# Kernel tuning notes

Measured on AMD Instinct MI355X. Metric: run time of the kernel, lower is better.

The kernel has to match this reference:

```python
import jax, jax.numpy as jnp
import numpy as np

B_, H_, N_, L_ = 4, 512, 64, 2048  # batch, d_model, d_state/2 (conj pairs), seq len


def setup_inputs() -> dict:
    key = jax.random.key(0)
    ks = jax.random.split(key, 8)
    x = jax.random.normal(ks[0], (B_, H_, L_), jnp.float32)
    ln_w = jnp.ones((H_,), jnp.float32)
    ln_b = jnp.zeros((H_,), jnp.float32)
    # S4D-style init: dt log-uniform in [1e-3, 1e-1], A = -1/2 + i*pi*n (S4D-Lin)
    log_dt = jax.random.uniform(ks[1], (H_,), jnp.float32) * (np.log(0.1) - np.log(0.001)) + np.log(0.001)
    log_A_real = jnp.broadcast_to(jnp.log(jnp.float32(0.5)), (H_, N_))
    A_imag = jnp.broadcast_to(np.pi * jnp.arange(N_, dtype=np.float32), (H_, N_))
    B_re = jnp.ones((H_, N_), jnp.float32)
    B_im = jnp.zeros((H_, N_), jnp.float32)
    # 2 kernel channels for bidirectional
    C_re = jax.random.normal(ks[2], (2, H_, N_), jnp.float32) * (0.5 ** 0.5)
    C_im = jax.random.normal(ks[3], (2, H_, N_), jnp.float32) * (0.5 ** 0.5)
    D = jax.random.normal(ks[4], (H_,), jnp.float32)
    W_out = jax.random.normal(ks[5], (H_, H_), jnp.float32) / np.sqrt(H_)
    b_out = jnp.zeros((H_,), jnp.float32)
    return dict(x=x, ln_w=ln_w, ln_b=ln_b, log_dt=log_dt, log_A_real=log_A_real,
                A_imag=A_imag, B_re=B_re, B_im=B_im, C_re=C_re, C_im=C_im,
                D=D, W_out=W_out, b_out=b_out)


def _s4_layer(x, ln_w, ln_b, log_dt, log_A_real, A_imag, B_re, B_im, C_re, C_im, D, W_out, b_out):
    Bb, H, L = x.shape
    # ---- pre-norm LayerNorm over channel dim (module transposes to (B,L,H)) ----
    zt = x.transpose(0, 2, 1)                          # (B, L, H)
    mu = zt.mean(-1, keepdims=True)
    var = jnp.mean((zt - mu) ** 2, -1, keepdims=True)
    zt = (zt - mu) * jax.lax.rsqrt(var + 1e-5) * ln_w + ln_b
    z = zt.transpose(0, 2, 1)                          # (B, H, L)
    # ---- S4 diagonal SSM kernel, ZOH discretization, 2 channels (bidirectional) ----
    dt = jnp.exp(log_dt)[:, None]                      # (H, 1)
    A = -jnp.exp(log_A_real) + 1j * A_imag             # (H, N)
    dtA = A * dt                                       # (H, N)
    dB = (B_re + 1j * B_im) * (jnp.exp(dtA) - 1.0) / A # (H, N) discretized B
    CB = (C_re + 1j * C_im) * dB                       # (2, H, N)
    V = jnp.exp(dtA[:, :, None] * jnp.arange(L))       # (H, N, L) Vandermonde exp(l*dt*A)
    k = 2.0 * jnp.real(jnp.einsum('chn,hnl->chl', CB, V))  # (2, H, L)
    # ---- bidirectional: causal + flipped anticausal kernel, length 2L ----
    zpad = jnp.zeros_like(k[0])
    kb = jnp.concatenate([k[0], zpad], -1) + jnp.concatenate([zpad, k[1][:, ::-1]], -1)  # (H, 2L)
    # ---- FFT convolution ----
    k_f = jnp.fft.rfft(kb, n=2 * L)                    # (H, L+1)
    u_f = jnp.fft.rfft(z, n=2 * L)                     # (B, H, L+1)
    y = jnp.fft.irfft(u_f * k_f, n=2 * L)[..., :L]     # (B, H, L)
    y = y + z * D[:, None]                             # skip connection D*u
    y = jax.nn.gelu(y)                                 # default S4 activation
    y = jnp.einsum('oh,bhl->bol', W_out, y) + b_out[:, None]  # output linear (Conv1d k=1)
    return y + x                                       # residual of S4Layer


def reference(x, ln_w, ln_b, log_dt, log_A_real, A_imag, B_re, B_im, C_re, C_im, D, W_out, b_out):
    return _s4_layer(x, ln_w, ln_b, log_dt, log_A_real, A_imag, B_re, B_im, C_re, C_im, D, W_out, b_out)
```

## Files before the change

### kernel.cpp

```cpp
#include <hip/hip_runtime.h>
#include <math.h>

#define Bq 4
#define Hq 512
#define Nq 64
#define Lq 2048
#define PARAM (Hq*Nq)
#define T 64
#define NC (Lq/T)
#define NCOL 256

__global__ void prep_kernel(const float* __restrict__ log_dt,
                            const float* __restrict__ log_A_real,
                            const float* __restrict__ A_imag,
                            const float* __restrict__ B_re, const float* __restrict__ B_im,
                            const float* __restrict__ C_re, const float* __restrict__ C_im,
                            float* __restrict__ a0, float* __restrict__ b0,
                            float* __restrict__ a1, float* __restrict__ b1,
                            float* __restrict__ pw) {
    int idx = blockIdx.x * blockDim.x + threadIdx.x;
    if (idx >= PARAM) return;
    int h = idx >> 6, n = idx & 63;
    float dt = expf(log_dt[h]);
    float Ar = -expf(log_A_real[idx]);
    float Ai = A_imag[idx];
    float er = expf(Ar * dt);
    float wr = er * cosf(Ai * dt);
    float wi = er * sinf(Ai * dt);
    float mr = wr - 1.0f, mi = wi;
    float den = Ar * Ar + Ai * Ai;
    float qr = (mr * Ar + mi * Ai) / den;
    float qi = (mi * Ar - mr * Ai) / den;
    float Br = B_re[idx], Bi = B_im[idx];
    float dBr = Br * qr - Bi * qi;
    float dBi = Br * qi + Bi * qr;
    float cr = C_re[idx], ci = C_im[idx];
    a0[idx] =  2.0f * (cr * dBr - ci * dBi);
    b0[idx] = -2.0f * (cr * dBi + ci * dBr);
    cr = C_re[PARAM + idx]; ci = C_im[PARAM + idx];
    a1[idx] =  2.0f * (cr * dBr - ci * dBi);
    b1[idx] = -2.0f * (cr * dBi + ci * dBr);
    float c = 1.f, s = 0.f;
    float* base = pw + (size_t)h * 65 * 128 + 2 * n;
    for (int d = 0; d <= 64; ++d) {
        *(float2*)(base + (size_t)d * 128) = float2{c, s};
        float nc = c * wr - s * wi;
        float ns = c * wi + s * wr;
        c = nc; s = ns;
    }
}

__global__ __launch_bounds__(128)
void ktap_kernel(const float* __restrict__ pw,
                 const float* __restrict__ a0, const float* __restrict__ b0,
                 const float* __restrict__ a1, const float* __restrict__ b1,
                 float* __restrict__ kt) {
    int h = blockIdx.x;
    int t = threadIdx.x;
    int dir = t >> 6, d = t & 63;
    const float* aa = dir ? a1 : a0;
    const float* bb = dir ? b1 : b0;
    const float* row = pw + (size_t)(h * 65 + d) * 128;
    float acc = 0.f;
    for (int n = 0; n < 64; ++n) {
        float2 v = *(const float2*)(row + 2 * n);
        acc = fmaf(aa[h * 64 + n], v.x, acc);
        acc = fmaf(bb[h * 64 + n], v.y, acc);
    }
    kt[((size_t)h * 2 + dir) * 64 + d] = acc;
}

__global__ __launch_bounds__(256)
void ln_kernel(const float* __restrict__ x, const float* __restrict__ lnw,
               const float* __restrict__ lnb, float* __restrict__ z) {
    int blk = blockIdx.x;
    int b  = blk / (Lq / 16);
    int l0 = (blk % (Lq / 16)) * 16;
    int tx = threadIdx.x & 15;
    int ty = threadIdx.x >> 4;
    const float* xb = x + (size_t)b * Hq * Lq;
    float s = 0.f, s2 = 0.f;
    for (int h = ty; h < Hq; h += 16) {
        float v = xb[h * Lq + l0 + tx];
        s += v; s2 += v * v;
    }
    __shared__ float rs_[16][17], r2_[16][17], mu_s[16], sg_s[16];
    rs_[ty][tx] = s; r2_[ty][tx] = s2;
    __syncthreads();
    if (ty == 0) {
        float a = 0.f, c = 0.f;
        #pragma unroll
        for (int i = 0; i < 16; ++i) { a += rs_[i][tx]; c += r2_[i][tx]; }
        float mu = a * (1.0f / Hq);
        float var = c * (1.0f / Hq) - mu * mu;
        mu_s[tx] = mu;
        sg_s[tx] = rsqrtf(var + 1e-5f);
    }
    __syncthreads();
    float mu = mu_s[tx], rs = sg_s[tx];
    float* zb = z + (size_t)b * Hq * Lq;
    for (int h = ty; h < Hq; h += 16) {
        float v = xb[h * Lq + l0 + tx];
        zb[h * Lq + l0 + tx] = (v - mu) * rs * lnw[h] + lnb[h];
    }
}

__global__ __launch_bounds__(256, 6)
void delta_kernel(const float* __restrict__ z, const float* __restrict__ pw,
                  float* __restrict__ buf) {
    __shared__ float Bs[64][68];
    int h = blockIdx.x, ct = blockIdx.y;
    int t = threadIdx.x;
    int dir = ct >> 1;
    int cc = t & 31, rb = (t >> 5) & 1, jg = t >> 6;
    int b = (ct & 1) * 2 + rb;
    const float* zb = z + ((size_t)b * Hq + h) * Lq;
    if (dir == 0) {
        #pragma unroll
        for (int f = 0; f < 4; ++f) {
            float4 v = *(const float4*)(zb + cc * 64 + 16 * jg + 4 * f);
            Bs[16*jg+4*f+0][rb*32+cc] = v.x;
            Bs[16*jg+4*f+1][rb*32+cc] = v.y;
            Bs[16*jg+4*f+2][rb*32+cc] = v.z;
            Bs[16*jg+4*f+3][rb*32+cc] = v.w;
        }
    } else {
        #pragma unroll
        for (int f = 0; f < 4; ++f) {
            float4 v = *(const float4*)(zb + 2044 - cc * 64 - 16 * jg - 4 * f);
            Bs[16*jg+4*f+3][rb*32+cc] = v.x;
            Bs[16*jg+4*f+2][rb*32+cc] = v.y;
            Bs[16*jg+4*f+1][rb*32+cc] = v.z;
            Bs[16*jg+4*f+0][rb*32+cc] = v.w;
        }
    }
    __syncthreads();
    int tx = t & 15, ty = t >> 4;
    float aR[4][4] = {}, aI[4][4] = {};
    const float* pwh = pw + (size_t)h * 65 * 128;
    #pragma unroll 4
    for (int kk = 0; kk < 64; ++kk) {
        int d = 63 - kk;
        const float4* pr = (const float4*)(pwh + (size_t)d * 128 + 8 * tx);
        float4 p0 = pr[0], p1 = pr[1];
        float4 bv = *(const float4*)&Bs[kk][4 * ty];
        float pc[4] = {p0.x, p0.z, p1.x, p1.z};
        float ps[4] = {p0.y, p0.w, p1.y, p1.w};
        #pragma unroll
        for (int rr = 0; rr < 4; ++rr) {
            #pragma unroll
            for (int q = 0; q < 4; ++q) {
                aR[rr][q] = fmaf(pc[rr], (&bv.x)[q], aR[rr][q]);
                aI[rr][q] = fmaf(ps[rr], (&bv.x)[q], aI[rr][q]);
            }
        }
    }
    #pragma unroll
    for (int q = 0; q < 4; ++q) {
        int colg = ct * 64 + 4 * ty + q;
        float* dst = buf + ((size_t)h * NCOL + colg) * 128 + 8 * tx;
        float4 v1, v2;
        v1.x = aR[0][q]; v1.y = aI[0][q]; v1.z = aR[1][q]; v1.w = aI[1][q];
        v2.x = aR[2][q]; v2.y = aI[2][q]; v2.z = aR[3][q]; v2.w = aI[3][q];
        *(float4*)dst = v1; *(float4*)(dst + 4) = v2;
    }
}

__global__ __launch_bounds__(256)
void cscan_kernel(const float* __restrict__ pw, float* __restrict__ buf) {
    int e = blockIdx.x * 4 + (threadIdx.x >> 6);
    int n = threadIdx.x & 63;
    int h = e >> 3, dir = (e >> 2) & 1, b = e & 3;
    float2 t64 = *(const float2*)(pw + (size_t)(h * 65 + 64) * 128 + 2 * n);
    float tc = t64.x, ts = t64.y;
    float sr = 0.f, si = 0.f;
    float2* p = (float2*)(buf + ((size_t)h * NCOL + dir * 128 + b * 32) * 128) + n;
    float2 d = p[0];
    for (int c = 0; c < NC; ++c) {
        float2 dn;
        if (c + 1 < NC) dn = p[(c + 1) * 64];
        float2 s; s.x = sr; s.y = si;
        p[c * 64] = s;
        float nr = fmaf(tc, sr, fmaf(-ts, si, d.x));
        float ni = fmaf(ts, sr, fmaf(tc, si, d.y));
        sr = nr; si = ni; d = dn;
    }
}

__global__ __launch_bounds__(256, 8)
void yact_kernel(const float* __restrict__ z, const float* __restrict__ pw,
                 const float* __restrict__ a0, const float* __restrict__ b0,
                 const float* __restrict__ a1, const float* __restrict__ b1,
                 const float* __restrict__ kt, const float* __restrict__ buf,
                 const float* __restrict__ Dv, float* __restrict__ u) {
    __shared__ float As[32][68];
    __shared__ float Bs[32][36];
    __shared__ float ks0[64], ks1[64], as0_[64], bs0_[64], as1_[64], bs1_[64];
    int h = blockIdx.x, b = blockIdx.y;
    int t = threadIdx.x;
    if (t < 64) {
        ks0[t]  = kt[((size_t)h * 2 + 0) * 64 + t];
        ks1[t]  = kt[((size_t)h * 2 + 1) * 64 + t];
        as0_[t] = a0[h * 64 + t]; bs0_[t] = b0[h * 64 + t];
        as1_[t] = a1[h * 64 + t]; bs1_[t] = b1[h * 64 + t];
    }
    int tx = t & 15, ty = t >> 4;
    int si = t & 63, kkg = t >> 6;
    int cc = t & 31, kg = t >> 5;
    const float* zb   = z + ((size_t)b * Hq + h) * Lq;
    const float* bufh = buf + (size_t)h * NCOL * 128;
    const float* prow0 = pw + (size_t)(h * 65 + si + 1) * 128;
    const float* prow1 = pw + (size_t)(h * 65 + 63 - si) * 128;
    float acc[4][2] = {};
    __syncthreads();
    for (int p = 0; p < 10; ++p) {
        if (p < 2) {
            #pragma unroll
            for (int q = 0; q < 8; ++q) {
                int kk = 8 * kkg + q;
                int j = 32 * p + kk;
                int d = si - j;
                As[kk][si] = (d >= 0) ? ks0[d] : ks1[-d - 1];
            }
        } else if (p < 6) {
            #pragma unroll
            for (int q = 0; q < 8; ++q) {
                int kk = 8 * kkg + q;
                int m = 32 * (p - 2) + kk;
                int n = m >> 1;
                float2 v = *(const float2*)(prow0 + 2 * n);
                As[kk][si] = ((m & 1) == 0) ? fmaf(as0_[n], v.x, bs0_[n] * v.y)
                                            : fmaf(bs0_[n], v.x, -as0_[n] * v.y);
            }
        } else {
            #pragma unroll
            for (int q = 0; q < 8; ++q) {
                int kk = 8 * kkg + q;
                int m = 32 * (p - 6) + kk;
                int n = m >> 1;
                float2 v = *(const float2*)(prow1 + 2 * n);
                As[kk][si] = ((m & 1) == 0) ? fmaf(as1_[n], v.x, bs1_[n] * v.y)
                                            : fmaf(bs1_[n], v.x, -as1_[n] * v.y);
            }
        }
        if (p < 2) {
            float4 v = *(const float4*)(zb + cc * 64 + 32 * p + 4 * kg);
            Bs[4*kg+0][cc] = v.x; Bs[4*kg+1][cc] = v.y;
            Bs[4*kg+2][cc] = v.z; Bs[4*kg+3][cc] = v.w;
        } else if (p < 6) {
            int colg = b * 32 + cc;
            float4 v = *(const float4*)(bufh + (size_t)colg * 128 + 32 * (p - 2) + 4 * kg);
            Bs[4*kg+0][cc] = v.x; Bs[4*kg+1][cc] = v.y;
            Bs[4*kg+2][cc] = v.z; Bs[4*kg+3][cc] = v.w;
        } else {
            int colg = 128 + b * 32 + (31 - cc);
            float4 v = *(const float4*)(bufh + (size_t)colg * 128 + 32 * (p - 6) + 4 * kg);
            Bs[4*kg+0][cc] = v.x; Bs[4*kg+1][cc] = v.y;
            Bs[4*kg+2][cc] = v.z; Bs[4*kg+3][cc] = v.w;
        }
        __syncthreads();
        #pragma unroll 8
        for (int kk = 0; kk < 32; ++kk) {
            float4 av = *(const float4*)&As[kk][4 * tx];
            float2 bv = *(const float2*)&Bs[kk][2 * ty];
            #pragma unroll
            for (int ii = 0; ii < 4; ++ii) {
                float a = (&av.x)[ii];
                acc[ii][0] = fmaf(a, bv.x, acc[ii][0]);
                acc[ii][1] = fmaf(a, bv.y, acc[ii][1]);
            }
        }
        __syncthreads();
    }
    float dv = Dv[h];
    #pragma unroll
    for (int q = 0; q < 2; ++q) {
        int cc2 = 2 * ty + q;
        size_t base = ((size_t)b * Hq + h) * Lq + cc2 * 64 + 4 * tx;
        float4 zr = *(const float4*)(z + base);
        float vv[4];
        vv[0] = acc[0][q] + dv * zr.x;
        vv[1] = acc[1][q] + dv * zr.y;
        vv[2] = acc[2][q] + dv * zr.z;
        vv[3] = acc[3][q] + dv * zr.w;
        #pragma unroll
        for (int i = 0; i < 4; ++i) {
            float v = vv[i];
            float tt = tanhf(0.7978845608028654f * (v + 0.044715f * v * v * v));
            vv[i] = 0.5f * v * (1.0f + tt);
        }
        float4 r; r.x = vv[0]; r.y = vv[1]; r.z = vv[2]; r.w = vv[3];
        *(float4*)(u + base) = r;
    }
}

__global__ __launch_bounds__(512, 4)
void gemm_kernel(const float* __restrict__ u, const float* __restrict__ W,
                 const float* __restrict__ bias, const float* __restrict__ x,
                 float* __restrict__ out) {
    int l0 = blockIdx.x * 64;
    int o0 = blockIdx.y * 128;
    int b  = blockIdx.z;
    int tid = threadIdx.x;
    __shared__ float Ws[2][32][132];
    __shared__ float Us[2][32][68];
    const float* ub = u + (size_t)b * Hq * Lq;
    float acc[4][4] = {};
    int wo = tid >> 4, wl = tid & 15;
    int sj = tid & 31, so = tid >> 5;
    int sl = tid & 63, sk = tid >> 6;
    float wreg[8], ureg[4];
    #pragma unroll
    for (int r = 0; r < 8; ++r) wreg[r] = W[(size_t)(o0 + so + 16*r) * Hq + sj];
    #pragma unroll
    for (int r = 0; r < 4; ++r) ureg[r] = ub[(size_t)(4*sk + r) * Lq + l0 + sl];
    #pragma unroll
    for (int r = 0; r < 8; ++r) Ws[0][sj][so + 16*r] = wreg[r];
    #pragma unroll
    for (int r = 0; r < 4; ++r) Us[0][4*sk + r][sl] = ureg[r];
    __syncthreads();
    for (int t = 0; t < Hq / 32; ++t) {
        int cur = t & 1;
        if (t < 15) {
            int k0 = (t + 1) * 32;
            #pragma unroll
            for (int r = 0; r < 8; ++r)
                wreg[r] = W[(size_t)(o0 + so + 16*r) * Hq + k0 + sj];
            #pragma unroll
            for (int r = 0; r < 4; ++r)
                ureg[r] = ub[(size_t)(k0 + 4*sk + r) * Lq + l0 + sl];
        }
        #pragma unroll 8
        for (int j = 0; j < 32; ++j) {
            float4 av = *(const float4*)&Ws[cur][j][4 * wo];
            float4 bv = *(const float4*)&Us[cur][j][4 * wl];
            #pragma unroll
            for (int io = 0; io < 4; ++io) {
                float a = (&av.x)[io];
                acc[io][0] = fmaf(a, bv.x, acc[io][0]);
                acc[io][1] = fmaf(a, bv.y, acc[io][1]);
                acc[io][2] = fmaf(a, bv.z, acc[io][2]);
                acc[io][3] = fmaf(a, bv.w, acc[io][3]);
            }
        }
        if (t < 15) {
            int nxt = cur ^ 1;
            #pragma unroll
            for (int r = 0; r < 8; ++r) Ws[nxt][sj][so + 16*r] = wreg[r];
            #pragma unroll
            for (int r = 0; r < 4; ++r) Us[nxt][4*sk + r][sl] = ureg[r];
        }
        __syncthreads();
    }
    #pragma unroll
    for (int io = 0; io < 4; ++io) {
        int o = o0 + 4 * wo + io;
        float bo = bias[o];
        size_t base = ((size_t)b * Hq + o) * Lq + l0 + 4 * wl;
        const float4 xr = *(const float4*)(x + base);
        float4 r;
        r.x = acc[io][0] + bo + xr.x;
        r.y = acc[io][1] + bo + xr.y;
        r.z = acc[io][2] + bo + xr.z;
        r.w = acc[io][3] + bo + xr.w;
        *(float4*)(out + base) = r;
    }
}

extern "C" void kernel_launch(void* const* d_in, const int* in_sizes, int n_in,
                              void* d_out, int out_size, void* d_ws, size_t ws_size,
                              hipStream_t stream) {
    (void)in_sizes; (void)n_in; (void)out_size; (void)ws_size;
    const float* x          = (const float*)d_in[0];
    const float* ln_w       = (const float*)d_in[1];
    const float* ln_b       = (const float*)d_in[2];
    const float* log_dt     = (const float*)d_in[3];
    const float* log_A_real = (const float*)d_in[4];
    const float* A_imag     = (const float*)d_in[5];
    const float* B_re       = (const float*)d_in[6];
    const float* B_im       = (const float*)d_in[7];
    const float* C_re       = (const float*)d_in[8];
    const float* C_im       = (const float*)d_in[9];
    const float* Dv         = (const float*)d_in[10];
    const float* W          = (const float*)d_in[11];
    const float* b_out      = (const float*)d_in[12];
    float* out = (float*)d_out;
    float* ws  = (float*)d_ws;

    const size_t BHL = (size_t)Bq * Hq * Lq;
    float* a0  = ws;
    float* b0  = ws + (size_t)PARAM;
    float* a1  = ws + 2 * (size_t)PARAM;
    float* b1  = ws + 3 * (size_t)PARAM;
    float* kt  = ws + 4 * (size_t)PARAM;
    float* pw  = ws + 6 * (size_t)PARAM;
    float* z   = ws + 136 * (size_t)PARAM;
    float* u   = z  + BHL;
    float* buf = u + BHL;

    prep_kernel<<<PARAM / 256, 256, 0, stream>>>(log_dt, log_A_real, A_imag,
                                                 B_re, B_im, C_re, C_im,
                                                 a0, b0, a1, b1, pw);
    ln_kernel<<<Bq * (Lq / 16), 256, 0, stream>>>(x, ln_w, ln_b, z);
    ktap_kernel<<<Hq, 128, 0, stream>>>(pw, a0, b0, a1, b1, kt);
    delta_kernel<<<dim3(Hq, 4), 256, 0, stream>>>(z, pw, buf);
    cscan_kernel<<<Bq * Hq * 2 / 4, 256, 0, stream>>>(pw, buf);
    yact_kernel<<<dim3(Hq, Bq), 256, 0, stream>>>(z, pw, a0, b0, a1, b1,
                                                  kt, buf, Dv, u);
    gemm_kernel<<<dim3(Lq / 64, Hq / 128, Bq), 512, 0, stream>>>(u, W, b_out, x, out);
}
```

Before: 325.1 us.

## Enlarge yact tile to two batches, prefetch operands into registers, transpose power table

The yact kernel now covers two batches per block (64 columns) with a 64-deep k-step, so each thread computes a 4x4 micro-tile instead of 4x2. This halves the grid and the number of sync-separated phases. The next phase's B operands and power-table values are loaded into registers while the current tile is being computed. A transposed copy of the power table is written in prep so the per-thread reads are contiguous. The cost is larger shared memory, more registers, fewer blocks (occupancy hint lowered to 4), and extra writes in prep.

```diff
diff --git a/kernel.cpp b/kernel.cpp
--- a/kernel.cpp
+++ b/kernel.cpp
@@ -17,7 +17,7 @@
                             const float* __restrict__ C_re, const float* __restrict__ C_im,
                             float* __restrict__ a0, float* __restrict__ b0,
                             float* __restrict__ a1, float* __restrict__ b1,
-                            float* __restrict__ pw) {
+                            float* __restrict__ pw, float* __restrict__ pwT) {
     int idx = blockIdx.x * blockDim.x + threadIdx.x;
     if (idx >= PARAM) return;
     int h = idx >> 6, n = idx & 63;
@@ -41,9 +41,11 @@
     a1[idx] =  2.0f * (cr * dBr - ci * dBi);
     b1[idx] = -2.0f * (cr * dBi + ci * dBr);
     float c = 1.f, s = 0.f;
-    float* base = pw + (size_t)h * 65 * 128 + 2 * n;
+    float* base  = pw  + (size_t)h * 65 * 128 + 2 * n;
+    float* baseT = pwT + (size_t)(h * 64 + n) * 132;
     for (int d = 0; d <= 64; ++d) {
         *(float2*)(base + (size_t)d * 128) = float2{c, s};
+        *(float2*)(baseT + 2 * d)          = float2{c, s};
         float nc = c * wr - s * wi;
         float ns = c * wi + s * wr;
         c = nc; s = ns;
@@ -187,16 +189,16 @@
     }
 }
 
-__global__ __launch_bounds__(256, 8)
-void yact_kernel(const float* __restrict__ z, const float* __restrict__ pw,
+__global__ __launch_bounds__(256, 4)
+void yact_kernel(const float* __restrict__ z, const float* __restrict__ pwT,
                  const float* __restrict__ a0, const float* __restrict__ b0,
                  const float* __restrict__ a1, const float* __restrict__ b1,
                  const float* __restrict__ kt, const float* __restrict__ buf,
                  const float* __restrict__ Dv, float* __restrict__ u) {
-    __shared__ float As[32][68];
-    __shared__ float Bs[32][36];
+    __shared__ float As[64][68];
+    __shared__ float Bs[64][68];
     __shared__ float ks0[64], ks1[64], as0_[64], bs0_[64], as1_[64], bs1_[64];
-    int h = blockIdx.x, b = blockIdx.y;
+    int h = blockIdx.x, bp = blockIdx.y;
     int t = threadIdx.x;
     if (t < 64) {
         ks0[t]  = kt[((size_t)h * 2 + 0) * 64 + t];
@@ -205,78 +207,85 @@
         as1_[t] = a1[h * 64 + t]; bs1_[t] = b1[h * 64 + t];
     }
     int tx = t & 15, ty = t >> 4;
-    int si = t & 63, kkg = t >> 6;
-    int cc = t & 31, kg = t >> 5;
-    const float* zb   = z + ((size_t)b * Hq + h) * Lq;
+    int si = t & 63, kg = t >> 6;
+    int bS = 2 * bp + (si >> 5), ch = si & 31;
+    const float* zb   = z + ((size_t)bS * Hq + h) * Lq + ch * 64;
     const float* bufh = buf + (size_t)h * NCOL * 128;
-    const float* prow0 = pw + (size_t)(h * 65 + si + 1) * 128;
-    const float* prow1 = pw + (size_t)(h * 65 + 63 - si) * 128;
-    float acc[4][2] = {};
+    const float* buf0 = bufh + (size_t)(bS * 32 + ch) * 128;
+    const float* buf1 = bufh + (size_t)(128 + bS * 32 + (31 - ch)) * 128;
+    const float* pwh  = pwT + (size_t)h * 64 * 132;
+    float4 rB[4];
+    float2 pv[8];
+    #pragma unroll
+    for (int f = 0; f < 4; ++f)
+        rB[f] = *(const float4*)(zb + 16 * kg + 4 * f);
+    float acc[4][4] = {};
     __syncthreads();
-    for (int p = 0; p < 10; ++p) {
-        if (p < 2) {
-            #pragma unroll
-            for (int q = 0; q < 8; ++q) {
-                int kk = 8 * kkg + q;
-                int j = 32 * p + kk;
-                int d = si - j;
+    for (int p = 0; p < 5; ++p) {
+        if (p == 0) {
+            #pragma unroll
+            for (int q = 0; q < 16; ++q) {
+                int kk = 16 * kg + q;
+                int d = si - kk;
                 As[kk][si] = (d >= 0) ? ks0[d] : ks1[-d - 1];
             }
-        } else if (p < 6) {
-            #pragma unroll
-            for (int q = 0; q < 8; ++q) {
-                int kk = 8 * kkg + q;
-                int m = 32 * (p - 2) + kk;
-                int n = m >> 1;
-                float2 v = *(const float2*)(prow0 + 2 * n);
-                As[kk][si] = ((m & 1) == 0) ? fmaf(as0_[n], v.x, bs0_[n] * v.y)
-                                            : fmaf(bs0_[n], v.x, -as0_[n] * v.y);
-            }
         } else {
-            #pragma unroll
-            for (int q = 0; q < 8; ++q) {
-                int kk = 8 * kkg + q;
-                int m = 32 * (p - 6) + kk;
-                int n = m >> 1;
-                float2 v = *(const float2*)(prow1 + 2 * n);
-                As[kk][si] = ((m & 1) == 0) ? fmaf(as1_[n], v.x, bs1_[n] * v.y)
-                                            : fmaf(bs1_[n], v.x, -as1_[n] * v.y);
-            }
-        }
-        if (p < 2) {
-            float4 v = *(const float4*)(zb + cc * 64 + 32 * p + 4 * kg);
-            Bs[4*kg+0][cc] = v.x; Bs[4*kg+1][cc] = v.y;
-            Bs[4*kg+2][cc] = v.z; Bs[4*kg+3][cc] = v.w;
-        } else if (p < 6) {
-            int colg = b * 32 + cc;
-            float4 v = *(const float4*)(bufh + (size_t)colg * 128 + 32 * (p - 2) + 4 * kg);
-            Bs[4*kg+0][cc] = v.x; Bs[4*kg+1][cc] = v.y;
-            Bs[4*kg+2][cc] = v.z; Bs[4*kg+3][cc] = v.w;
-        } else {
-            int colg = 128 + b * 32 + (31 - cc);
-            float4 v = *(const float4*)(bufh + (size_t)colg * 128 + 32 * (p - 6) + 4 * kg);
-            Bs[4*kg+0][cc] = v.x; Bs[4*kg+1][cc] = v.y;
-            Bs[4*kg+2][cc] = v.z; Bs[4*kg+3][cc] = v.w;
+            const float* as_ = (p < 3) ? as0_ : as1_;
+            const float* bs_ = (p < 3) ? bs0_ : bs1_;
+            int pp = (p < 3) ? (p - 1) : (p - 3);
+            #pragma unroll
+            for (int q = 0; q < 16; ++q) {
+                int j = q >> 1;
+                int n = 32 * pp + 8 * kg + j;
+                float vx = pv[j].x, vy = pv[j].y;
+                As[16 * kg + q][si] = ((q & 1) == 0)
+                    ? fmaf(as_[n], vx, bs_[n] * vy)
+                    : fmaf(bs_[n], vx, -as_[n] * vy);
+            }
+        }
+        #pragma unroll
+        for (int f = 0; f < 4; ++f) {
+            Bs[16*kg + 4*f + 0][si] = rB[f].x;
+            Bs[16*kg + 4*f + 1][si] = rB[f].y;
+            Bs[16*kg + 4*f + 2][si] = rB[f].z;
+            Bs[16*kg + 4*f + 3][si] = rB[f].w;
         }
         __syncthreads();
+        if (p < 4) {
+            int pn = p + 1;
+            int pp = (pn < 3) ? (pn - 1) : (pn - 3);
+            const float* src = (pn < 3) ? buf0 : buf1;
+            #pragma unroll
+            for (int f = 0; f < 4; ++f)
+                rB[f] = *(const float4*)(src + 64 * pp + 16 * kg + 4 * f);
+            int dsel = (pn < 3) ? (si + 1) : (63 - si);
+            #pragma unroll
+            for (int j = 0; j < 8; ++j) {
+                int n = 32 * pp + 8 * kg + j;
+                pv[j] = *(const float2*)(pwh + (size_t)n * 132 + 2 * dsel);
+            }
+        }
         #pragma unroll 8
-        for (int kk = 0; kk < 32; ++kk) {
+        for (int kk = 0; kk < 64; ++kk) {
             float4 av = *(const float4*)&As[kk][4 * tx];
-            float2 bv = *(const float2*)&Bs[kk][2 * ty];
+            float4 bv = *(const float4*)&Bs[kk][4 * ty];
             #pragma unroll
             for (int ii = 0; ii < 4; ++ii) {
                 float a = (&av.x)[ii];
                 acc[ii][0] = fmaf(a, bv.x, acc[ii][0]);
                 acc[ii][1] = fmaf(a, bv.y, acc[ii][1]);
+                acc[ii][2] = fmaf(a, bv.z, acc[ii][2]);
+                acc[ii][3] = fmaf(a, bv.w, acc[ii][3]);
             }
         }
         __syncthreads();
     }
     float dv = Dv[h];
     #pragma unroll
-    for (int q = 0; q < 2; ++q) {
-        int cc2 = 2 * ty + q;
-        size_t base = ((size_t)b * Hq + h) * Lq + cc2 * 64 + 4 * tx;
+    for (int q = 0; q < 4; ++q) {
+        int cc2 = 4 * ty + q;
+        int b2 = 2 * bp + (cc2 >> 5), ch2 = cc2 & 31;
+        size_t base = ((size_t)b2 * Hq + h) * Lq + ch2 * 64 + 4 * tx;
         float4 zr = *(const float4*)(z + base);
         float vv[4];
         vv[0] = acc[0][q] + dv * zr.x;
@@ -394,18 +403,19 @@
     float* b1  = ws + 3 * (size_t)PARAM;
     float* kt  = ws + 4 * (size_t)PARAM;
     float* pw  = ws + 6 * (size_t)PARAM;
-    float* z   = ws + 136 * (size_t)PARAM;
+    float* pwT = ws + 136 * (size_t)PARAM;
+    float* z   = ws + 268 * (size_t)PARAM;
     float* u   = z  + BHL;
     float* buf = u + BHL;
 
     prep_kernel<<<PARAM / 256, 256, 0, stream>>>(log_dt, log_A_real, A_imag,
                                                  B_re, B_im, C_re, C_im,
-                                                 a0, b0, a1, b1, pw);
+                                                 a0, b0, a1, b1, pw, pwT);
     ln_kernel<<<Bq * (Lq / 16), 256, 0, stream>>>(x, ln_w, ln_b, z);
     ktap_kernel<<<Hq, 128, 0, stream>>>(pw, a0, b0, a1, b1, kt);
     delta_kernel<<<dim3(Hq, 4), 256, 0, stream>>>(z, pw, buf);
     cscan_kernel<<<Bq * Hq * 2 / 4, 256, 0, stream>>>(pw, buf);
-    yact_kernel<<<dim3(Hq, Bq), 256, 0, stream>>>(z, pw, a0, b0, a1, b1,
-                                                  kt, buf, Dv, u);
+    yact_kernel<<<dim3(Hq, 2), 256, 0, stream>>>(z, pwT, a0, b0, a1, b1,
+                                                 kt, buf, Dv, u);
     gemm_kernel<<<dim3(Lq / 64, Hq / 128, Bq), 512, 0, stream>>>(u, W, b_out, x, out);
 }
```

Result: faster. 316.3 us (-2.7%).
